# Optimization experiments

Measured on AMD Instinct MI355X. Metric: run time of the kernel, lower is better.

Reference implementation:

```python
import jax, jax.numpy as jnp
import numpy as np

SHAPES = np.array([[64, 64], [32, 32], [16, 16], [8, 8]], dtype=np.int64)  # (H_l, W_l)
STARTS = np.array([0, 4096, 5120, 5376], dtype=np.int64)
N_HEADS, N_LEVELS, N_POINTS = 8, 4, 4
NUM_LAYERS, D_MODEL, D_FFN = 6, 256, 1024
B, S = 1, int(SHAPES[:, 0].dot(SHAPES[:, 1]).item()) if False else (1, 5440)[1]
B = 1


def setup_inputs():
    key = jax.random.key(0)
    ks = jax.random.split(key, 16)
    C, F, L = D_MODEL, D_FFN, NUM_LAYERS
    w = lambda k, shape, s: jax.random.normal(k, shape, jnp.float32) * s
    d = {}
    d["src"] = jax.random.normal(ks[0], (B, S, C), jnp.float32)
    d["pos"] = jax.random.normal(ks[1], (B, S, C), jnp.float32) * 0.1
    d["valid_ratios"] = jnp.ones((B, N_LEVELS, 2), jnp.float32)
    d["spatial_shapes"] = jnp.asarray(SHAPES)
    d["level_start_index"] = jnp.asarray(STARTS)
    d["Wv"] = w(ks[2], (L, C, C), 0.03); d["bv"] = jnp.zeros((L, C), jnp.float32)
    d["Woff"] = w(ks[3], (L, C, N_HEADS * N_LEVELS * N_POINTS * 2), 0.002)
    d["boff"] = w(ks[4], (L, N_HEADS * N_LEVELS * N_POINTS * 2), 0.5)
    d["Wattn"] = w(ks[5], (L, C, N_HEADS * N_LEVELS * N_POINTS), 0.02)
    d["battn"] = jnp.zeros((L, N_HEADS * N_LEVELS * N_POINTS), jnp.float32)
    d["Wout"] = w(ks[6], (L, C, C), 0.03); d["bout"] = jnp.zeros((L, C), jnp.float32)
    d["ln1_g"] = jnp.ones((L, C), jnp.float32); d["ln1_b"] = jnp.zeros((L, C), jnp.float32)
    d["W1"] = w(ks[7], (L, C, F), 0.03); d["b1"] = jnp.zeros((L, F), jnp.float32)
    d["W2"] = w(ks[8], (L, F, C), 0.03); d["b2"] = jnp.zeros((L, C), jnp.float32)
    d["ln2_g"] = jnp.ones((L, C), jnp.float32); d["ln2_b"] = jnp.zeros((L, C), jnp.float32)
    return d


def layer_norm(x, g, b, eps=1e-5):
    m = jnp.mean(x, -1, keepdims=True)
    v = jnp.mean(jnp.square(x - m), -1, keepdims=True)
    return (x - m) * jax.lax.rsqrt(v + eps) * g + b


def get_reference_points(valid_ratios):
    # returns [B, S, L, 2] (x, y) normalized coords, matching the TF while-loop
    refs = []
    for l in range(N_LEVELS):
        H, W = int(SHAPES[l, 0]), int(SHAPES[l, 1])
        ry = jnp.linspace(0.5, H - 0.5, H)
        rx = jnp.linspace(0.5, W - 0.5, W)
        yy, xx = jnp.meshgrid(ry, rx, indexing='ij')
        yn = yy.reshape(-1)[None, :] / (valid_ratios[:, l, 0:1] * H)
        xn = xx.reshape(-1)[None, :] / (valid_ratios[:, l, 1:2] * W)
        refs.append(jnp.stack([xn, yn], -1))  # [B, H*W, 2]
    ref = jnp.concatenate(refs, axis=1)       # [B, S, 2]
    vr_wh = valid_ratios[:, None, :, ::-1]    # [B, 1, L, 2] -> (w, h)
    return ref[:, :, None, :] * vr_wh


def bilinear_sample(v_l, loc, Hl, Wl):
    # v_l: [B, Hl*Wl, nH, Dh]; loc: [B, S, nH, P, 2] in [0,1] coords
    # grid_sample align_corners=False, zero padding: pix = loc*size - 0.5
    x = loc[..., 0] * Wl - 0.5
    y = loc[..., 1] * Hl - 0.5
    x0 = jnp.floor(x); y0 = jnp.floor(y)
    lx = x - x0; ly = y - y0
    x0i = x0.astype(jnp.int32); y0i = y0.astype(jnp.int32)
    b_idx = jnp.arange(v_l.shape[0])[:, None, None, None]
    h_idx = jnp.arange(v_l.shape[2])[None, None, :, None]

    def gather(xi, yi):
        valid = (xi >= 0) & (xi < Wl) & (yi >= 0) & (yi < Hl)
        idx = jnp.clip(yi, 0, Hl - 1) * Wl + jnp.clip(xi, 0, Wl - 1)
        v = v_l[b_idx, idx, h_idx, :]  # [B,S,nH,P,Dh]
        return v * valid[..., None].astype(v.dtype)

    v00 = gather(x0i, y0i); v01 = gather(x0i + 1, y0i)
    v10 = gather(x0i, y0i + 1); v11 = gather(x0i + 1, y0i + 1)
    w00 = (1 - lx) * (1 - ly); w01 = lx * (1 - ly)
    w10 = (1 - lx) * ly; w11 = lx * ly
    return (v00 * w00[..., None] + v01 * w01[..., None]
            + v10 * w10[..., None] + v11 * w11[..., None])


def msda(query, src, ref, Wv, bv, Woff, boff, Wattn, battn, Wout, bout):
    Bq, Sq, C = src.shape
    Dh = C // N_HEADS
    value = (src @ Wv + bv).reshape(Bq, Sq, N_HEADS, Dh)
    off = (query @ Woff + boff).reshape(Bq, Sq, N_HEADS, N_LEVELS, N_POINTS, 2)
    aw = jax.nn.softmax((query @ Wattn + battn)
                        .reshape(Bq, Sq, N_HEADS, N_LEVELS * N_POINTS), -1)
    aw = aw.reshape(Bq, Sq, N_HEADS, N_LEVELS, N_POINTS)
    normalizer = jnp.asarray(SHAPES[:, ::-1].copy(), jnp.float32)  # [L,2]=(W,H)
    loc = ref[:, :, None, :, None, :] + off / normalizer[None, None, None, :, None, :]
    out = jnp.zeros((Bq, Sq, N_HEADS, Dh), value.dtype)
    for l in range(N_LEVELS):
        Hl, Wl = int(SHAPES[l, 0]), int(SHAPES[l, 1])
        s0 = int(STARTS[l])
        v_l = value[:, s0:s0 + Hl * Wl]
        sampled = bilinear_sample(v_l, loc[:, :, :, l], Hl, Wl)  # [B,S,nH,P,Dh]
        out = out + jnp.einsum('bshpd,bshp->bshd', sampled, aw[:, :, :, l])
    return out.reshape(Bq, Sq, C) @ Wout + bout


def reference(src, pos, valid_ratios, spatial_shapes, level_start_index,
              Wv, bv, Woff, boff, Wattn, battn, Wout, bout,
              ln1_g, ln1_b, W1, b1, W2, b2, ln2_g, ln2_b):
    ref = get_reference_points(valid_ratios)
    x = src
    for i in range(NUM_LAYERS):
        a = msda(x + pos, x, ref, Wv[i], bv[i], Woff[i], boff[i],
                 Wattn[i], battn[i], Wout[i], bout[i])
        x = layer_norm(x + a, ln1_g[i], ln1_b[i])
        f = jax.nn.relu(x @ W1[i] + b1[i]) @ W2[i] + b2[i]
        x = layer_norm(x + f, ln2_g[i], ln2_b[i])
    return x
```

## Files before the change

### kernel.cpp

```cpp
#include <hip/hip_runtime.h>
#include <hip/hip_bf16.h>

#define S_TOT 5440
#define C_DIM 256
#define F_DIM 1024
#define N_LAYERS 6

__device__ __constant__ int c_HW[4]    = {64, 32, 16, 8};
__device__ __constant__ int c_logW[4]  = {6, 5, 4, 3};
__device__ __constant__ int c_start[4] = {0, 4096, 5120, 5376};

typedef __attribute__((ext_vector_type(8))) short bf16x8;
typedef __attribute__((ext_vector_type(4))) float f32x4;

__device__ __forceinline__ short f2bf(float f) {
    __hip_bfloat16 h = __float2bfloat16(f);
    return *reinterpret_cast<short*>(&h);
}

__global__ __launch_bounds__(256) void prep_weights(
    const float* __restrict__ Wv, const float* __restrict__ Woff,
    const float* __restrict__ Wattn, const float* __restrict__ Wout,
    const float* __restrict__ W1, const float* __restrict__ W2,
    unsigned short* __restrict__ WT)
{
    __shared__ short T[64][72];
    const int bid = blockIdx.x;
    const int layer = bid / 184;
    const int r = bid % 184;
    const float* src; unsigned short* dst; int K, N, kb, nb;
    if (r < 16)       { src = Wv    + (long)layer*65536;  dst = WT + 0       + (long)layer*65536;  K=256;  N=256;  kb=r&3;        nb=r>>2; }
    else if (r < 32)  { src = Woff  + (long)layer*65536;  dst = WT + 393216  + (long)layer*65536;  K=256;  N=256;  kb=(r-16)&3;   nb=(r-16)>>2; }
    else if (r < 40)  { src = Wattn + (long)layer*32768;  dst = WT + 786432  + (long)layer*32768;  K=256;  N=128;  kb=(r-32)&3;   nb=(r-32)>>2; }
    else if (r < 56)  { src = Wout  + (long)layer*65536;  dst = WT + 983040  + (long)layer*65536;  K=256;  N=256;  kb=(r-40)&3;   nb=(r-40)>>2; }
    else if (r < 120) { src = W1    + (long)layer*262144; dst = WT + 1376256 + (long)layer*262144; K=256;  N=1024; kb=(r-56)&3;   nb=(r-56)>>2; }
    else              { src = W2    + (long)layer*262144; dst = WT + 2949120 + (long)layer*262144; K=1024; N=256;  kb=(r-120)&15; nb=(r-120)>>4; }
    const int k0 = kb * 64, n0 = nb * 64;
    const int t = threadIdx.x;
    {
        const int row = t >> 2, cg = (t & 3) * 16;
        const float* sp = src + (long)(k0 + row) * N + n0 + cg;
        float4 v0 = *(const float4*)sp;
        float4 v1 = *(const float4*)(sp + 4);
        float4 v2 = *(const float4*)(sp + 8);
        float4 v3 = *(const float4*)(sp + 12);
        short tmp[16];
        tmp[0]=f2bf(v0.x); tmp[1]=f2bf(v0.y); tmp[2]=f2bf(v0.z); tmp[3]=f2bf(v0.w);
        tmp[4]=f2bf(v1.x); tmp[5]=f2bf(v1.y); tmp[6]=f2bf(v1.z); tmp[7]=f2bf(v1.w);
        tmp[8]=f2bf(v2.x); tmp[9]=f2bf(v2.y); tmp[10]=f2bf(v2.z); tmp[11]=f2bf(v2.w);
        tmp[12]=f2bf(v3.x); tmp[13]=f2bf(v3.y); tmp[14]=f2bf(v3.z); tmp[15]=f2bf(v3.w);
        *(bf16x8*)&T[row][cg]     = *(bf16x8*)&tmp[0];
        *(bf16x8*)&T[row][cg + 8] = *(bf16x8*)&tmp[8];
    }
    __syncthreads();
    {
        const int n = t >> 2, kg = (t & 3) * 16;
        short o[16];
        #pragma unroll
        for (int j = 0; j < 16; ++j) o[j] = T[kg + j][n];
        unsigned short* dp = dst + (long)(n0 + n) * K + k0 + kg;
        *(bf16x8*)dp       = *(bf16x8*)&o[0];
        *(bf16x8*)(dp + 8) = *(bf16x8*)&o[8];
    }
}

__global__ __launch_bounds__(256) void prep_x0(
    const float* __restrict__ src, const float* __restrict__ pos,
    unsigned short* __restrict__ x_bf, unsigned short* __restrict__ xp_bf)
{
    const long i = ((long)blockIdx.x * 256 + threadIdx.x) * 4;
    float4 s = *(const float4*)(src + i);
    float4 p = *(const float4*)(pos + i);
    ushort4 a, b;
    a.x = f2bf(s.x); a.y = f2bf(s.y); a.z = f2bf(s.z); a.w = f2bf(s.w);
    b.x = f2bf(s.x + p.x); b.y = f2bf(s.y + p.y); b.z = f2bf(s.z + p.z); b.w = f2bf(s.w + p.w);
    *(ushort4*)(x_bf + i) = a;
    *(ushort4*)(xp_bf + i) = b;
}

struct Acc { f32x4 a[2][4]; };

__device__ __forceinline__ void gemm_core_bf(
    const unsigned short* __restrict__ A, const unsigned short* __restrict__ Bt,
    int K, int mBase, int nBase, short (*As)[72], short (*Bs)[72], Acc& acc)
{
    const int t = threadIdx.x;
    const int lane = t & 63;
    const int wave = t >> 6;
    const int wr = wave >> 1, wc = wave & 1;
    const int lr = lane & 15;

    #pragma unroll
    for (int i = 0; i < 2; ++i)
        #pragma unroll
        for (int j = 0; j < 4; ++j)
            acc.a[i][j] = (f32x4){0.f, 0.f, 0.f, 0.f};

    for (int k0 = 0; k0 < K; k0 += 64) {
        bf16x8 ra[2], rb[4];
        #pragma unroll
        for (int q = 0; q < 2; ++q) {
            int flat = q * 256 + t, row = flat >> 3, cg = (flat & 7) * 8;
            ra[q] = *(const bf16x8*)(A + (long)(mBase + row) * K + k0 + cg);
        }
        #pragma unroll
        for (int q = 0; q < 4; ++q) {
            int flat = q * 256 + t, row = flat >> 3, cg = (flat & 7) * 8;
            rb[q] = *(const bf16x8*)(Bt + (long)(nBase + row) * K + k0 + cg);
        }
        __syncthreads();
        #pragma unroll
        for (int q = 0; q < 2; ++q) {
            int flat = q * 256 + t, row = flat >> 3, cg = (flat & 7) * 8;
            *(bf16x8*)&As[row][cg] = ra[q];
        }
        #pragma unroll
        for (int q = 0; q < 4; ++q) {
            int flat = q * 256 + t, row = flat >> 3, cg = (flat & 7) * 8;
            *(bf16x8*)&Bs[row][cg] = rb[q];
        }
        __syncthreads();
        #pragma unroll
        for (int kk = 0; kk < 2; ++kk) {
            const int lk = kk * 32 + (lane >> 4) * 8;
            bf16x8 af[2], bfr[4];
            #pragma unroll
            for (int fm = 0; fm < 2; ++fm)
                af[fm] = *(bf16x8*)&As[wr * 32 + fm * 16 + lr][lk];
            #pragma unroll
            for (int fn = 0; fn < 4; ++fn)
                bfr[fn] = *(bf16x8*)&Bs[wc * 64 + fn * 16 + lr][lk];
            #pragma unroll
            for (int fm = 0; fm < 2; ++fm)
                #pragma unroll
                for (int fn = 0; fn < 4; ++fn)
                    acc.a[fm][fn] = __builtin_amdgcn_mfma_f32_16x16x32_bf16(
                        af[fm], bfr[fn], acc.a[fm][fn], 0, 0, 0);
        }
    }
}

__global__ __launch_bounds__(256) void gemm_bf(
    const unsigned short* __restrict__ A, const unsigned short* __restrict__ Bt,
    const float* __restrict__ bias, const float* __restrict__ res,
    float* __restrict__ outF, unsigned short* __restrict__ outB,
    int K, int N, int relu)
{
    __shared__ short As[64][72];
    __shared__ short Bs[128][72];
    const int mBase = blockIdx.x * 64, nBase = blockIdx.y * 128;
    Acc acc;
    gemm_core_bf(A, Bt, K, mBase, nBase, As, Bs, acc);

    const int lane = threadIdx.x & 63;
    const int wave = threadIdx.x >> 6;
    const int wr = wave >> 1, wc = wave & 1;
    #pragma unroll
    for (int fm = 0; fm < 2; ++fm)
        #pragma unroll
        for (int fn = 0; fn < 4; ++fn)
            #pragma unroll
            for (int r = 0; r < 4; ++r) {
                int m = mBase + wr * 32 + fm * 16 + (lane >> 4) * 4 + r;
                int n = nBase + wc * 64 + fn * 16 + (lane & 15);
                float v = acc.a[fm][fn][r] + bias[n];
                if (res)  v += res[(long)m * N + n];
                if (relu) v = fmaxf(v, 0.f);
                if (outF) outF[(long)m * N + n] = v;
                if (outB) outB[(long)m * N + n] = (unsigned short)f2bf(v);
            }
}

__global__ __launch_bounds__(256) void proj_bf(
    const unsigned short* __restrict__ x_bf, const unsigned short* __restrict__ xp_bf,
    const unsigned short* __restrict__ WvT, const float* __restrict__ bv,
    const unsigned short* __restrict__ WofT, const float* __restrict__ bof,
    const unsigned short* __restrict__ WatT, const float* __restrict__ bat,
    float* __restrict__ value, float* __restrict__ offraw, float* __restrict__ logits)
{
    __shared__ short As[64][72];
    __shared__ short Bs[128][72];
    const int ny = blockIdx.y;
    const unsigned short* Ap; const unsigned short* Bp;
    const float* bias; float* out; int Nout, nb;
    if (ny < 2)      { Ap = x_bf;  Bp = WvT;  bias = bv;  out = value;  Nout = 256; nb = ny; }
    else if (ny < 4) { Ap = xp_bf; Bp = WofT; bias = bof; out = offraw; Nout = 256; nb = ny - 2; }
    else             { Ap = xp_bf; Bp = WatT; bias = bat; out = logits; Nout = 128; nb = 0; }
    const int mBase = blockIdx.x * 64, nBase = nb * 128;

    Acc acc;
    gemm_core_bf(Ap, Bp, 256, mBase, nBase, As, Bs, acc);

    const int lane = threadIdx.x & 63;
    const int wave = threadIdx.x >> 6;
    const int wr = wave >> 1, wc = wave & 1;
    #pragma unroll
    for (int fm = 0; fm < 2; ++fm)
        #pragma unroll
        for (int fn = 0; fn < 4; ++fn)
            #pragma unroll
            for (int r = 0; r < 4; ++r) {
                int m = mBase + wr * 32 + fm * 16 + (lane >> 4) * 4 + r;
                int n = nBase + wc * 64 + fn * 16 + (lane & 15);
                out[(long)m * Nout + n] = acc.a[fm][fn][r] + bias[n];
            }
}

__global__ __launch_bounds__(256) void msda_sample(
    const float* __restrict__ value, const float* __restrict__ offraw,
    const float* __restrict__ logits, const float* __restrict__ vr,
    unsigned short* __restrict__ outB)
{
    const int s = blockIdx.x;
    const int t = threadIdx.x;

    __shared__ int4   sIdx[128];
    __shared__ float4 sW[128];
    __shared__ float4 sPart[192];

    if (t < 128) {
        const int pt = t & 15;
        const int l = pt >> 2;

        float lg = logits[s * 128 + t];
        float m = lg;
        #pragma unroll
        for (int o = 1; o < 16; o <<= 1) m = fmaxf(m, __shfl_xor(m, o));
        float e = expf(lg - m);
        float sum = e;
        #pragma unroll
        for (int o = 1; o < 16; o <<= 1) sum += __shfl_xor(sum, o);
        float aw = e / sum;

        int ls = (s < 4096) ? 0 : (s < 5120) ? 1 : (s < 5376) ? 2 : 3;
        int lw = c_logW[ls];
        int Wq = c_HW[ls];
        int rem = s - c_start[ls];
        int qi = rem >> lw, qj = rem & (Wq - 1);
        float xh = (qj + 0.5f) / (vr[ls * 2 + 1] * (float)Wq);
        float yh = (qi + 0.5f) / (vr[ls * 2 + 0] * (float)Wq);

        const int Wl = c_HW[l], sl = c_start[l];
        const float fW = (float)Wl;
        float refx = xh * vr[l * 2 + 1];
        float refy = yh * vr[l * 2 + 0];
        float ox = offraw[s * 256 + t * 2];
        float oy = offraw[s * 256 + t * 2 + 1];
        float x = refx * fW + ox - 0.5f;
        float y = refy * fW + oy - 0.5f;
        float x0f = floorf(x), y0f = floorf(y);
        float fx = x - x0f, fy = y - y0f;
        int x0 = (int)x0f, y0 = (int)y0f;
        int x1 = x0 + 1, y1 = y0 + 1;
        float vx0 = (x0 >= 0 && x0 < Wl) ? 1.f : 0.f;
        float vx1 = (x1 >= 0 && x1 < Wl) ? 1.f : 0.f;
        float vy0 = (y0 >= 0 && y0 < Wl) ? 1.f : 0.f;
        float vy1 = (y1 >= 0 && y1 < Wl) ? 1.f : 0.f;
        int cx0 = min(max(x0, 0), Wl - 1), cx1 = min(max(x1, 0), Wl - 1);
        int cy0 = min(max(y0, 0), Wl - 1), cy1 = min(max(y1, 0), Wl - 1);

        int4 id;
        id.x = sl + cy0 * Wl + cx0;
        id.y = sl + cy0 * Wl + cx1;
        id.z = sl + cy1 * Wl + cx0;
        id.w = sl + cy1 * Wl + cx1;
        sIdx[t] = id;
        float4 w4;
        w4.x = aw * (1.f - fx) * (1.f - fy) * vx0 * vy0;
        w4.y = aw * fx * (1.f - fy) * vx1 * vy0;
        w4.z = aw * (1.f - fx) * fy * vx0 * vy1;
        w4.w = aw * fx * fy * vx1 * vy1;
        sW[t] = w4;
    }
    __syncthreads();

    const int pg = t >> 6;
    const int h  = (t >> 3) & 7;
    const int dq = t & 7;
    const int cb = h * 32 + dq * 4;

    f32x4 acc = (f32x4){0.f, 0.f, 0.f, 0.f};
    #pragma unroll
    for (int p = 0; p < 4; ++p) {
        const int e = h * 16 + pg * 4 + p;
        int4 id = sIdx[e];
        float4 w = sW[e];
        f32x4 v0 = *(const f32x4*)(value + id.x * 256 + cb);
        f32x4 v1 = *(const f32x4*)(value + id.y * 256 + cb);
        f32x4 v2 = *(const f32x4*)(value + id.z * 256 + cb);
        f32x4 v3 = *(const f32x4*)(value + id.w * 256 + cb);
        acc += w.x * v0 + w.y * v1 + w.z * v2 + w.w * v3;
    }

    if (pg > 0) {
        float4 st; st.x = acc[0]; st.y = acc[1]; st.z = acc[2]; st.w = acc[3];
        sPart[(pg - 1) * 64 + (t & 63)] = st;
    }
    __syncthreads();
    if (pg == 0) {
        float4 p0 = sPart[t], p1 = sPart[64 + t], p2 = sPart[128 + t];
        acc[0] += p0.x + p1.x + p2.x;
        acc[1] += p0.y + p1.y + p2.y;
        acc[2] += p0.z + p1.z + p2.z;
        acc[3] += p0.w + p1.w + p2.w;
        ushort4 o;
        o.x = (unsigned short)f2bf(acc[0]);
        o.y = (unsigned short)f2bf(acc[1]);
        o.z = (unsigned short)f2bf(acc[2]);
        o.w = (unsigned short)f2bf(acc[3]);
        *(ushort4*)(outB + (long)s * 256 + cb) = o;
    }
}

__global__ __launch_bounds__(256) void ln4(
    const float* __restrict__ in, const float* __restrict__ g,
    const float* __restrict__ b, float* __restrict__ outF,
    unsigned short* __restrict__ outB, const float* __restrict__ pos,
    unsigned short* __restrict__ outXp)
{
    const int wave = threadIdx.x >> 6, lane = threadIdx.x & 63;
    const int s = blockIdx.x * 4 + wave;
    f32x4 v = *(const f32x4*)(in + (long)s * 256 + lane * 4);

    float sum = v[0] + v[1] + v[2] + v[3];
    #pragma unroll
    for (int o = 1; o < 64; o <<= 1) sum += __shfl_xor(sum, o);
    const float mean = sum * (1.f / 256.f);

    f32x4 d = v - mean;
    float sq = d[0]*d[0] + d[1]*d[1] + d[2]*d[2] + d[3]*d[3];
    #pragma unroll
    for (int o = 1; o < 64; o <<= 1) sq += __shfl_xor(sq, o);
    const float rstd = rsqrtf(sq * (1.f / 256.f) + 1e-5f);

    f32x4 gg = *(const f32x4*)(g + lane * 4);
    f32x4 bb = *(const f32x4*)(b + lane * 4);
    f32x4 o4 = d * rstd * gg + bb;
    outF[(long)s * 256 + lane * 4 + 0] = o4[0];
    outF[(long)s * 256 + lane * 4 + 1] = o4[1];
    outF[(long)s * 256 + lane * 4 + 2] = o4[2];
    outF[(long)s * 256 + lane * 4 + 3] = o4[3];
    if (outB) {
        ushort4 ob;
        ob.x = (unsigned short)f2bf(o4[0]); ob.y = (unsigned short)f2bf(o4[1]);
        ob.z = (unsigned short)f2bf(o4[2]); ob.w = (unsigned short)f2bf(o4[3]);
        *(ushort4*)(outB + (long)s * 256 + lane * 4) = ob;
    }
    if (outXp) {
        f32x4 p = *(const f32x4*)(pos + (long)s * 256 + lane * 4);
        f32x4 xp = o4 + p;
        ushort4 op;
        op.x = (unsigned short)f2bf(xp[0]); op.y = (unsigned short)f2bf(xp[1]);
        op.z = (unsigned short)f2bf(xp[2]); op.w = (unsigned short)f2bf(xp[3]);
        *(ushort4*)(outXp + (long)s * 256 + lane * 4) = op;
    }
}

extern "C" void kernel_launch(void* const* d_in, const int* in_sizes, int n_in,
                              void* d_out, int out_size, void* d_ws, size_t ws_size,
                              hipStream_t stream) {
    const float* src   = (const float*)d_in[0];
    const float* pos   = (const float*)d_in[1];
    const float* vr    = (const float*)d_in[2];
    const float* Wv    = (const float*)d_in[5];
    const float* bv    = (const float*)d_in[6];
    const float* Woff  = (const float*)d_in[7];
    const float* boff  = (const float*)d_in[8];
    const float* Wattn = (const float*)d_in[9];
    const float* battn = (const float*)d_in[10];
    const float* Wout  = (const float*)d_in[11];
    const float* bout  = (const float*)d_in[12];
    const float* ln1g  = (const float*)d_in[13];
    const float* ln1b  = (const float*)d_in[14];
    const float* W1    = (const float*)d_in[15];
    const float* b1    = (const float*)d_in[16];
    const float* W2    = (const float*)d_in[17];
    const float* b2    = (const float*)d_in[18];
    const float* ln2g  = (const float*)d_in[19];
    const float* ln2b  = (const float*)d_in[20];

    const int S = S_TOT, C = C_DIM;
    const long SC = (long)S * C;

    float* ws     = (float*)d_ws;
    float* xbuf   = ws;
    float* tmp    = xbuf + SC;
    float* value  = tmp + SC;
    float* offraw = value + SC;
    float* logits = offraw + SC;
    float* fend   = logits + (long)S * 128;
    unsigned short* x_bf  = (unsigned short*)fend;
    unsigned short* xp_bf = x_bf + SC;
    unsigned short* WT    = xp_bf + SC;
    unsigned short* msda_bf = (unsigned short*)logits;
    unsigned short* hbuf_bf = (unsigned short*)value;

    const unsigned short* WvT = WT + 0;
    const unsigned short* WofT = WT + 393216;
    const unsigned short* WatT = WT + 786432;
    const unsigned short* WouT = WT + 983040;
    const unsigned short* W1T = WT + 1376256;
    const unsigned short* W2T = WT + 2949120;

    prep_weights<<<1104, 256, 0, stream>>>(Wv, Woff, Wattn, Wout, W1, W2, WT);
    prep_x0<<<1360, 256, 0, stream>>>(src, pos, x_bf, xp_bf);

    const float* x = src;
    for (int i = 0; i < N_LAYERS; ++i) {
        proj_bf<<<dim3(85, 5), 256, 0, stream>>>(
            x_bf, xp_bf,
            WvT + (long)i * 65536, bv + i * C,
            WofT + (long)i * 65536, boff + (long)i * 256,
            WatT + (long)i * 32768, battn + (long)i * 128,
            value, offraw, logits);

        msda_sample<<<S, 256, 0, stream>>>(value, offraw, logits, vr, msda_bf);

        gemm_bf<<<dim3(85, 2), 256, 0, stream>>>(
            msda_bf, WouT + (long)i * 65536, bout + i * C, x, tmp, nullptr, 256, 256, 0);

        ln4<<<S / 4, 256, 0, stream>>>(tmp, ln1g + i * C, ln1b + i * C, xbuf, x_bf, nullptr, nullptr);

        gemm_bf<<<dim3(85, 8), 256, 0, stream>>>(
            x_bf, W1T + (long)i * 262144, b1 + (long)i * F_DIM, nullptr, nullptr, hbuf_bf, 256, 1024, 1);

        gemm_bf<<<dim3(85, 2), 256, 0, stream>>>(
            hbuf_bf, W2T + (long)i * 262144, b2 + i * C, xbuf, tmp, nullptr, 1024, 256, 0);

        float* dst = (i == N_LAYERS - 1) ? (float*)d_out : xbuf;
        if (i == N_LAYERS - 1) {
            ln4<<<S / 4, 256, 0, stream>>>(tmp, ln2g + i * C, ln2b + i * C, dst, nullptr, nullptr, nullptr);
        } else {
            ln4<<<S / 4, 256, 0, stream>>>(tmp, ln2g + i * C, ln2b + i * C, dst, x_bf, pos, xp_bf);
        }
        x = xbuf;
    }
}
```

Measured before the change: 508.1 us.

## Fuse LayerNorm into full-row GEMM epilogues and store value projection in bf16

The standalone LayerNorm kernels are removed. The Wout and W2 GEMMs now each compute a full 256-column row tile and apply bias, residual and LayerNorm in their epilogue, using a shared-memory reduction across the two column waves. That epilogue also writes the bf16 copies of x and x+pos. The value projection is stored as bf16 to halve the gather traffic in the sampling kernel. The FFN1 GEMM uses a wider 256-column tile. The intent is to drop the float tmp round-trips and two launches per layer, at the cost of only 85 blocks in the fused GEMMs, which leaves most of the GPU idle, and slightly lower precision in the sampled values.

```diff
diff --git a/kernel.cpp b/kernel.cpp
--- a/kernel.cpp
+++ b/kernel.cpp
@@ -16,6 +16,9 @@
 __device__ __forceinline__ short f2bf(float f) {
     __hip_bfloat16 h = __float2bfloat16(f);
     return *reinterpret_cast<short*>(&h);
+}
+__device__ __forceinline__ float bf2f(unsigned short u) {
+    union { unsigned int i; float f; } c; c.i = ((unsigned int)u) << 16; return c.f;
 }
 
 __global__ __launch_bounds__(256) void prep_weights(
@@ -78,11 +81,11 @@
     *(ushort4*)(xp_bf + i) = b;
 }
 
-struct Acc { f32x4 a[2][4]; };
-
-__device__ __forceinline__ void gemm_core_bf(
+template<int NF>
+__device__ __forceinline__ void gemm_core(
     const unsigned short* __restrict__ A, const unsigned short* __restrict__ Bt,
-    int K, int mBase, int nBase, short (*As)[72], short (*Bs)[72], Acc& acc)
+    int K, int mBase, int nBase, short (*As)[72], short (*Bs)[72],
+    f32x4 (&acc)[2][NF])
 {
     const int t = threadIdx.x;
     const int lane = t & 63;
@@ -93,18 +96,18 @@
     #pragma unroll
     for (int i = 0; i < 2; ++i)
         #pragma unroll
-        for (int j = 0; j < 4; ++j)
-            acc.a[i][j] = (f32x4){0.f, 0.f, 0.f, 0.f};
+        for (int j = 0; j < NF; ++j)
+            acc[i][j] = (f32x4){0.f, 0.f, 0.f, 0.f};
 
     for (int k0 = 0; k0 < K; k0 += 64) {
-        bf16x8 ra[2], rb[4];
+        bf16x8 ra[2], rb[NF];
         #pragma unroll
         for (int q = 0; q < 2; ++q) {
             int flat = q * 256 + t, row = flat >> 3, cg = (flat & 7) * 8;
             ra[q] = *(const bf16x8*)(A + (long)(mBase + row) * K + k0 + cg);
         }
         #pragma unroll
-        for (int q = 0; q < 4; ++q) {
+        for (int q = 0; q < NF; ++q) {
             int flat = q * 256 + t, row = flat >> 3, cg = (flat & 7) * 8;
             rb[q] = *(const bf16x8*)(Bt + (long)(nBase + row) * K + k0 + cg);
         }
@@ -115,7 +118,7 @@
             *(bf16x8*)&As[row][cg] = ra[q];
         }
         #pragma unroll
-        for (int q = 0; q < 4; ++q) {
+        for (int q = 0; q < NF; ++q) {
             int flat = q * 256 + t, row = flat >> 3, cg = (flat & 7) * 8;
             *(bf16x8*)&Bs[row][cg] = rb[q];
         }
@@ -123,52 +126,21 @@
         #pragma unroll
         for (int kk = 0; kk < 2; ++kk) {
             const int lk = kk * 32 + (lane >> 4) * 8;
-            bf16x8 af[2], bfr[4];
+            bf16x8 af[2], bfr[NF];
             #pragma unroll
             for (int fm = 0; fm < 2; ++fm)
                 af[fm] = *(bf16x8*)&As[wr * 32 + fm * 16 + lr][lk];
             #pragma unroll
-            for (int fn = 0; fn < 4; ++fn)
-                bfr[fn] = *(bf16x8*)&Bs[wc * 64 + fn * 16 + lr][lk];
+            for (int fn = 0; fn < NF; ++fn)
+                bfr[fn] = *(bf16x8*)&Bs[wc * (NF * 16) + fn * 16 + lr][lk];
             #pragma unroll
             for (int fm = 0; fm < 2; ++fm)
                 #pragma unroll
-                for (int fn = 0; fn < 4; ++fn)
-                    acc.a[fm][fn] = __builtin_amdgcn_mfma_f32_16x16x32_bf16(
-                        af[fm], bfr[fn], acc.a[fm][fn], 0, 0, 0);
-        }
-    }
-}
-
-__global__ __launch_bounds__(256) void gemm_bf(
-    const unsigned short* __restrict__ A, const unsigned short* __restrict__ Bt,
-    const float* __restrict__ bias, const float* __restrict__ res,
-    float* __restrict__ outF, unsigned short* __restrict__ outB,
-    int K, int N, int relu)
-{
-    __shared__ short As[64][72];
-    __shared__ short Bs[128][72];
-    const int mBase = blockIdx.x * 64, nBase = blockIdx.y * 128;
-    Acc acc;
-    gemm_core_bf(A, Bt, K, mBase, nBase, As, Bs, acc);
-
-    const int lane = threadIdx.x & 63;
-    const int wave = threadIdx.x >> 6;
-    const int wr = wave >> 1, wc = wave & 1;
-    #pragma unroll
-    for (int fm = 0; fm < 2; ++fm)
-        #pragma unroll
-        for (int fn = 0; fn < 4; ++fn)
-            #pragma unroll
-            for (int r = 0; r < 4; ++r) {
-                int m = mBase + wr * 32 + fm * 16 + (lane >> 4) * 4 + r;
-                int n = nBase + wc * 64 + fn * 16 + (lane & 15);
-                float v = acc.a[fm][fn][r] + bias[n];
-                if (res)  v += res[(long)m * N + n];
-                if (relu) v = fmaxf(v, 0.f);
-                if (outF) outF[(long)m * N + n] = v;
-                if (outB) outB[(long)m * N + n] = (unsigned short)f2bf(v);
-            }
+                for (int fn = 0; fn < NF; ++fn)
+                    acc[fm][fn] = __builtin_amdgcn_mfma_f32_16x16x32_bf16(
+                        af[fm], bfr[fn], acc[fm][fn], 0, 0, 0);
+        }
+    }
 }
 
 __global__ __launch_bounds__(256) void proj_bf(
@@ -176,20 +148,21 @@
     const unsigned short* __restrict__ WvT, const float* __restrict__ bv,
     const unsigned short* __restrict__ WofT, const float* __restrict__ bof,
     const unsigned short* __restrict__ WatT, const float* __restrict__ bat,
-    float* __restrict__ value, float* __restrict__ offraw, float* __restrict__ logits)
+    unsigned short* __restrict__ value_bf, float* __restrict__ offraw,
+    float* __restrict__ logits)
 {
     __shared__ short As[64][72];
     __shared__ short Bs[128][72];
     const int ny = blockIdx.y;
     const unsigned short* Ap; const unsigned short* Bp;
-    const float* bias; float* out; int Nout, nb;
-    if (ny < 2)      { Ap = x_bf;  Bp = WvT;  bias = bv;  out = value;  Nout = 256; nb = ny; }
-    else if (ny < 4) { Ap = xp_bf; Bp = WofT; bias = bof; out = offraw; Nout = 256; nb = ny - 2; }
-    else             { Ap = xp_bf; Bp = WatT; bias = bat; out = logits; Nout = 128; nb = 0; }
+    const float* bias; int Nout, nb;
+    if (ny < 2)      { Ap = x_bf;  Bp = WvT;  bias = bv;  Nout = 256; nb = ny; }
+    else if (ny < 4) { Ap = xp_bf; Bp = WofT; bias = bof; Nout = 256; nb = ny - 2; }
+    else             { Ap = xp_bf; Bp = WatT; bias = bat; Nout = 128; nb = 0; }
     const int mBase = blockIdx.x * 64, nBase = nb * 128;
 
-    Acc acc;
-    gemm_core_bf(Ap, Bp, 256, mBase, nBase, As, Bs, acc);
+    f32x4 acc[2][4];
+    gemm_core<4>(Ap, Bp, 256, mBase, nBase, As, Bs, acc);
 
     const int lane = threadIdx.x & 63;
     const int wave = threadIdx.x >> 6;
@@ -202,12 +175,124 @@
             for (int r = 0; r < 4; ++r) {
                 int m = mBase + wr * 32 + fm * 16 + (lane >> 4) * 4 + r;
                 int n = nBase + wc * 64 + fn * 16 + (lane & 15);
-                out[(long)m * Nout + n] = acc.a[fm][fn][r] + bias[n];
-            }
+                float v = acc[fm][fn][r] + bias[n];
+                if (ny < 2) value_bf[(long)m * 256 + n] = (unsigned short)f2bf(v);
+                else if (ny < 4) offraw[(long)m * 256 + n] = v;
+                else logits[(long)m * 128 + n] = v;
+            }
+}
+
+__global__ __launch_bounds__(256) void gemm_relu(
+    const unsigned short* __restrict__ A, const unsigned short* __restrict__ Bt,
+    const float* __restrict__ bias, unsigned short* __restrict__ outB)
+{
+    __shared__ short As[64][72];
+    __shared__ short Bs[256][72];
+    const int mBase = blockIdx.x * 64, nBase = blockIdx.y * 256;
+    f32x4 acc[2][8];
+    gemm_core<8>(A, Bt, 256, mBase, nBase, As, Bs, acc);
+
+    const int lane = threadIdx.x & 63;
+    const int wave = threadIdx.x >> 6;
+    const int wr = wave >> 1, wc = wave & 1;
+    #pragma unroll
+    for (int fm = 0; fm < 2; ++fm)
+        #pragma unroll
+        for (int fn = 0; fn < 8; ++fn)
+            #pragma unroll
+            for (int r = 0; r < 4; ++r) {
+                int m = mBase + wr * 32 + fm * 16 + (lane >> 4) * 4 + r;
+                int n = nBase + wc * 128 + fn * 16 + (lane & 15);
+                float v = fmaxf(acc[fm][fn][r] + bias[n], 0.f);
+                outB[(long)m * 1024 + n] = (unsigned short)f2bf(v);
+            }
+}
+
+__global__ __launch_bounds__(256) void gemm_ln(
+    const unsigned short* __restrict__ A, const unsigned short* __restrict__ Bt,
+    const float* __restrict__ bias, const float* __restrict__ res,
+    const float* __restrict__ g, const float* __restrict__ b,
+    float* __restrict__ outF, unsigned short* __restrict__ outB,
+    const float* __restrict__ pos, unsigned short* __restrict__ outXp,
+    int K)
+{
+    __shared__ short As[64][72];
+    __shared__ short Bs[256][72];
+    __shared__ float2 sRed[2][64];
+    const int mBase = blockIdx.x * 64;
+    f32x4 acc[2][8];
+    gemm_core<8>(A, Bt, K, mBase, 0, As, Bs, acc);
+
+    const int lane = threadIdx.x & 63;
+    const int wave = threadIdx.x >> 6;
+    const int wr = wave >> 1, wc = wave & 1;
+    const int lc = lane & 15, lq = lane >> 4;
+
+    float g_c[8], b_c[8];
+    int ncol[8];
+    #pragma unroll
+    for (int fn = 0; fn < 8; ++fn) {
+        int n = wc * 128 + fn * 16 + lc;
+        ncol[fn] = n;
+        g_c[fn] = g[n];
+        b_c[fn] = b[n];
+    }
+
+    #pragma unroll
+    for (int fm = 0; fm < 2; ++fm)
+        #pragma unroll
+        for (int r = 0; r < 4; ++r) {
+            int m = mBase + wr * 32 + fm * 16 + lq * 4 + r;
+            #pragma unroll
+            for (int fn = 0; fn < 8; ++fn)
+                acc[fm][fn][r] += bias[ncol[fn]] + res[(long)m * 256 + ncol[fn]];
+        }
+
+    #pragma unroll
+    for (int fm = 0; fm < 2; ++fm)
+        #pragma unroll
+        for (int r = 0; r < 4; ++r) {
+            float s1 = 0.f, s2 = 0.f;
+            #pragma unroll
+            for (int fn = 0; fn < 8; ++fn) {
+                float vv = acc[fm][fn][r];
+                s1 += vv; s2 += vv * vv;
+            }
+            #pragma unroll
+            for (int o = 1; o < 16; o <<= 1) {
+                s1 += __shfl_xor(s1, o);
+                s2 += __shfl_xor(s2, o);
+            }
+            if (lc == 0) {
+                float2 pr; pr.x = s1; pr.y = s2;
+                sRed[wc][wr * 32 + fm * 16 + lq * 4 + r] = pr;
+            }
+        }
+    __syncthreads();
+
+    #pragma unroll
+    for (int fm = 0; fm < 2; ++fm)
+        #pragma unroll
+        for (int r = 0; r < 4; ++r) {
+            int row = wr * 32 + fm * 16 + lq * 4 + r;
+            float2 a0 = sRed[0][row], a1 = sRed[1][row];
+            float mean = (a0.x + a1.x) * (1.f / 256.f);
+            float var  = (a0.y + a1.y) * (1.f / 256.f) - mean * mean;
+            float rstd = rsqrtf(var + 1e-5f);
+            long mb = (long)(mBase + row) * 256;
+            #pragma unroll
+            for (int fn = 0; fn < 8; ++fn) {
+                float o = (acc[fm][fn][r] - mean) * rstd * g_c[fn] + b_c[fn];
+                outF[mb + ncol[fn]] = o;
+                if (outB) outB[mb + ncol[fn]] = (unsigned short)f2bf(o);
+                if (outXp) outXp[mb + ncol[fn]] =
+                    (unsigned short)f2bf(o + pos[mb + ncol[fn]]);
+            }
+        }
 }
 
 __global__ __launch_bounds__(256) void msda_sample(
-    const float* __restrict__ value, const float* __restrict__ offraw,
+    const unsigned short* __restrict__ value, const float* __restrict__ offraw,
     const float* __restrict__ logits, const float* __restrict__ vr,
     unsigned short* __restrict__ outB)
 {
@@ -285,10 +370,14 @@
         const int e = h * 16 + pg * 4 + p;
         int4 id = sIdx[e];
         float4 w = sW[e];
-        f32x4 v0 = *(const f32x4*)(value + id.x * 256 + cb);
-        f32x4 v1 = *(const f32x4*)(value + id.y * 256 + cb);
-        f32x4 v2 = *(const f32x4*)(value + id.z * 256 + cb);
-        f32x4 v3 = *(const f32x4*)(value + id.w * 256 + cb);
+        ushort4 u0 = *(const ushort4*)(value + id.x * 256 + cb);
+        ushort4 u1 = *(const ushort4*)(value + id.y * 256 + cb);
+        ushort4 u2 = *(const ushort4*)(value + id.z * 256 + cb);
+        ushort4 u3 = *(const ushort4*)(value + id.w * 256 + cb);
+        f32x4 v0 = (f32x4){bf2f(u0.x), bf2f(u0.y), bf2f(u0.z), bf2f(u0.w)};
+        f32x4 v1 = (f32x4){bf2f(u1.x), bf2f(u1.y), bf2f(u1.z), bf2f(u1.w)};
+        f32x4 v2 = (f32x4){bf2f(u2.x), bf2f(u2.y), bf2f(u2.z), bf2f(u2.w)};
+        f32x4 v3 = (f32x4){bf2f(u3.x), bf2f(u3.y), bf2f(u3.z), bf2f(u3.w)};
         acc += w.x * v0 + w.y * v1 + w.z * v2 + w.w * v3;
     }
 
@@ -309,50 +398,6 @@
         o.z = (unsigned short)f2bf(acc[2]);
         o.w = (unsigned short)f2bf(acc[3]);
         *(ushort4*)(outB + (long)s * 256 + cb) = o;
-    }
-}
-
-__global__ __launch_bounds__(256) void ln4(
-    const float* __restrict__ in, const float* __restrict__ g,
-    const float* __restrict__ b, float* __restrict__ outF,
-    unsigned short* __restrict__ outB, const float* __restrict__ pos,
-    unsigned short* __restrict__ outXp)
-{
-    const int wave = threadIdx.x >> 6, lane = threadIdx.x & 63;
-    const int s = blockIdx.x * 4 + wave;
-    f32x4 v = *(const f32x4*)(in + (long)s * 256 + lane * 4);
-
-    float sum = v[0] + v[1] + v[2] + v[3];
-    #pragma unroll
-    for (int o = 1; o < 64; o <<= 1) sum += __shfl_xor(sum, o);
-    const float mean = sum * (1.f / 256.f);
-
-    f32x4 d = v - mean;
-    float sq = d[0]*d[0] + d[1]*d[1] + d[2]*d[2] + d[3]*d[3];
-    #pragma unroll
-    for (int o = 1; o < 64; o <<= 1) sq += __shfl_xor(sq, o);
-    const float rstd = rsqrtf(sq * (1.f / 256.f) + 1e-5f);
-
-    f32x4 gg = *(const f32x4*)(g + lane * 4);
-    f32x4 bb = *(const f32x4*)(b + lane * 4);
-    f32x4 o4 = d * rstd * gg + bb;
-    outF[(long)s * 256 + lane * 4 + 0] = o4[0];
-    outF[(long)s * 256 + lane * 4 + 1] = o4[1];
-    outF[(long)s * 256 + lane * 4 + 2] = o4[2];
-    outF[(long)s * 256 + lane * 4 + 3] = o4[3];
-    if (outB) {
-        ushort4 ob;
-        ob.x = (unsigned short)f2bf(o4[0]); ob.y = (unsigned short)f2bf(o4[1]);
-        ob.z = (unsigned short)f2bf(o4[2]); ob.w = (unsigned short)f2bf(o4[3]);
-        *(ushort4*)(outB + (long)s * 256 + lane * 4) = ob;
-    }
-    if (outXp) {
-        f32x4 p = *(const f32x4*)(pos + (long)s * 256 + lane * 4);
-        f32x4 xp = o4 + p;
-        ushort4 op;
-        op.x = (unsigned short)f2bf(xp[0]); op.y = (unsigned short)f2bf(xp[1]);
-        op.z = (unsigned short)f2bf(xp[2]); op.w = (unsigned short)f2bf(xp[3]);
-        *(ushort4*)(outXp + (long)s * 256 + lane * 4) = op;
     }
 }
 
@@ -384,23 +429,21 @@
 
     float* ws     = (float*)d_ws;
     float* xbuf   = ws;
-    float* tmp    = xbuf + SC;
-    float* value  = tmp + SC;
-    float* offraw = value + SC;
+    float* offraw = xbuf + SC;
     float* logits = offraw + SC;
-    float* fend   = logits + (long)S * 128;
-    unsigned short* x_bf  = (unsigned short*)fend;
-    unsigned short* xp_bf = x_bf + SC;
-    unsigned short* WT    = xp_bf + SC;
-    unsigned short* msda_bf = (unsigned short*)logits;
-    unsigned short* hbuf_bf = (unsigned short*)value;
-
-    const unsigned short* WvT = WT + 0;
+    unsigned short* value_bf = (unsigned short*)(logits + (long)S * 128);
+    unsigned short* x_bf     = value_bf + SC;
+    unsigned short* xp_bf    = x_bf + SC;
+    unsigned short* msda_bf  = xp_bf + SC;
+    unsigned short* hbuf_bf  = msda_bf + SC;
+    unsigned short* WT       = hbuf_bf + (long)S * F_DIM;
+
+    const unsigned short* WvT  = WT + 0;
     const unsigned short* WofT = WT + 393216;
     const unsigned short* WatT = WT + 786432;
     const unsigned short* WouT = WT + 983040;
-    const unsigned short* W1T = WT + 1376256;
-    const unsigned short* W2T = WT + 2949120;
+    const unsigned short* W1T  = WT + 1376256;
+    const unsigned short* W2T  = WT + 2949120;
 
     prep_weights<<<1104, 256, 0, stream>>>(Wv, Woff, Wattn, Wout, W1, W2, WT);
     prep_x0<<<1360, 256, 0, stream>>>(src, pos, x_bf, xp_bf);
@@ -412,26 +455,26 @@
             WvT + (long)i * 65536, bv + i * C,
             WofT + (long)i * 65536, boff + (long)i * 256,
             WatT + (long)i * 32768, battn + (long)i * 128,
-            value, offraw, logits);
-
-        msda_sample<<<S, 256, 0, stream>>>(value, offraw, logits, vr, msda_bf);
-
-        gemm_bf<<<dim3(85, 2), 256, 0, stream>>>(
-            msda_bf, WouT + (long)i * 65536, bout + i * C, x, tmp, nullptr, 256, 256, 0);
-
-        ln4<<<S / 4, 256, 0, stream>>>(tmp, ln1g + i * C, ln1b + i * C, xbuf, x_bf, nullptr, nullptr);
-
-        gemm_bf<<<dim3(85, 8), 256, 0, stream>>>(
-            x_bf, W1T + (long)i * 262144, b1 + (long)i * F_DIM, nullptr, nullptr, hbuf_bf, 256, 1024, 1);
-
-        gemm_bf<<<dim3(85, 2), 256, 0, stream>>>(
-            hbuf_bf, W2T + (long)i * 262144, b2 + i * C, xbuf, tmp, nullptr, 1024, 256, 0);
-
-        float* dst = (i == N_LAYERS - 1) ? (float*)d_out : xbuf;
+            value_bf, offraw, logits);
+
+        msda_sample<<<S, 256, 0, stream>>>(value_bf, offraw, logits, vr, msda_bf);
+
+        gemm_ln<<<85, 256, 0, stream>>>(
+            msda_bf, WouT + (long)i * 65536, bout + i * C, x,
+            ln1g + i * C, ln1b + i * C, xbuf, x_bf, nullptr, nullptr, 256);
+
+        gemm_relu<<<dim3(85, 4), 256, 0, stream>>>(
+            x_bf, W1T + (long)i * 262144, b1 + (long)i * F_DIM, hbuf_bf);
+
         if (i == N_LAYERS - 1) {
-            ln4<<<S / 4, 256, 0, stream>>>(tmp, ln2g + i * C, ln2b + i * C, dst, nullptr, nullptr, nullptr);
+            gemm_ln<<<85, 256, 0, stream>>>(
+                hbuf_bf, W2T + (long)i * 262144, b2 + i * C, xbuf,
+                ln2g + i * C, ln2b + i * C, (float*)d_out,
+                nullptr, nullptr, nullptr, 1024);
         } else {
-            ln4<<<S / 4, 256, 0, stream>>>(tmp, ln2g + i * C, ln2b + i * C, dst, x_bf, pos, xp_bf);
+            gemm_ln<<<85, 256, 0, stream>>>(
+                hbuf_bf, W2T + (long)i * 262144, b2 + i * C, xbuf,
+                ln2g + i * C, ln2b + i * C, xbuf, x_bf, pos, xp_bf, 1024);
         }
         x = xbuf;
     }
```

New measurement: 529.7 us. 4.3% more time.
